# Kernel tuning notes

Measured on AMD Instinct MI355X. Metric: run time of the kernel, lower is better.

The kernel has to match this reference:

```python
import jax, jax.numpy as jnp
import numpy as np

H, HD, RD = 16, 128, 64          # n_heads, head_dim, rope_dim
CD = HD - RD                      # content_dim = 64
THETA = 10000.0


def apply_rope(x, cos, sin):
    # x: [B,H,T,RD]; cos/sin: [T,RD//2] broadcast over B,H
    d = x.shape[-1] // 2
    x1, x2 = x[..., :d], x[..., d:]
    return jnp.concatenate([x1 * cos - x2 * sin, x1 * sin + x2 * cos], axis=-1)


def setup_inputs() -> dict:
    key = jax.random.key(0)
    ks = jax.random.split(key, 9)
    d_model, q_rank, d_latent = 2048, 512, 512
    B, T = 2, 2048
    s = 0.02
    return {
        "x": jax.random.normal(ks[0], (B, T, d_model), dtype=jnp.float32),
        "Wq_down": jax.random.normal(ks[1], (d_model, q_rank), dtype=jnp.float32) * s,
        "Wq_up": jax.random.normal(ks[2], (q_rank, H * CD), dtype=jnp.float32) * s,
        "Wq_rope": jax.random.normal(ks[3], (d_model, H * RD), dtype=jnp.float32) * s,
        "Wkv_down": jax.random.normal(ks[4], (d_model, d_latent), dtype=jnp.float32) * s,
        "Wk_up": jax.random.normal(ks[5], (d_latent, H * CD), dtype=jnp.float32) * s,
        "Wv_up": jax.random.normal(ks[6], (d_latent, H * HD), dtype=jnp.float32) * s,
        "Wk_rope": jax.random.normal(ks[7], (d_model, H * RD), dtype=jnp.float32) * s,
        "Wo": jax.random.normal(ks[8], (H * HD, d_model), dtype=jnp.float32) * s,
    }


def reference(x, Wq_down, Wq_up, Wq_rope, Wkv_down, Wk_up, Wv_up, Wk_rope, Wo):
    B, T, _ = x.shape

    # low-rank projections
    q_content = (x @ Wq_down) @ Wq_up            # [B,T,H*CD]
    q_pos = x @ Wq_rope                          # [B,T,H*RD]
    kv_latent = x @ Wkv_down                     # [B,T,d_latent]
    k_content = kv_latent @ Wk_up                # [B,T,H*CD]
    k_pos = x @ Wk_rope                          # [B,T,H*RD]
    v = kv_latent @ Wv_up                        # [B,T,H*HD]

    def split_heads(t, d):
        return t.reshape(B, T, H, d).transpose(0, 2, 1, 3)  # [B,H,T,d]

    q_content = split_heads(q_content, CD)
    q_pos = split_heads(q_pos, RD)
    k_content = split_heads(k_content, CD)
    k_pos = split_heads(k_pos, RD)
    v = split_heads(v, HD)

    # rotary tables: [T, RD//2]
    inv_freq = 1.0 / (THETA ** (jnp.arange(0, RD, 2, dtype=jnp.float32) / RD))
    freqs = jnp.arange(T, dtype=jnp.float32)[:, None] * inv_freq[None, :]
    cos, sin = jnp.cos(freqs), jnp.sin(freqs)

    q_pos = apply_rope(q_pos, cos, sin)
    k_pos = apply_rope(k_pos, cos, sin)

    q = jnp.concatenate([q_content, q_pos], axis=-1)  # [B,H,T,HD]
    k = jnp.concatenate([k_content, k_pos], axis=-1)  # [B,H,T,HD]

    # causal SDPA, scale = 1/sqrt(head_dim)
    scale = 1.0 / jnp.sqrt(jnp.asarray(HD, dtype=q.dtype))
    scores = jnp.einsum("bhqd,bhkd->bhqk", q, k) * scale
    causal = jnp.tril(jnp.ones((T, T), dtype=bool))
    scores = jnp.where(causal, scores, jnp.finfo(scores.dtype).min)
    attn = jax.nn.softmax(scores, axis=-1)
    out = jnp.einsum("bhqk,bhkd->bhqd", attn, v)      # [B,H,T,HD]

    out = out.transpose(0, 2, 1, 3).reshape(B, T, H * HD)
    return out @ Wo
```

## Files before the change

kernel.cpp:

```cpp
#include <hip/hip_runtime.h>
#include <hip/hip_bf16.h>
#include <stdint.h>
#include <math.h>

#define H_ 16
#define HD_ 128
#define RD_ 64
#define CD_ 64
#define DM_ 2048
#define QR_ 512
#define DL_ 512
#define B_ 2
#define T_ 2048
#define M_TOT (B_*T_)

typedef __attribute__((ext_vector_type(8))) short short8;
typedef __attribute__((ext_vector_type(4))) float f32x4;
typedef __attribute__((ext_vector_type(16))) float f32x16;

__device__ __forceinline__ unsigned short f2b_hw(float f){
  __hip_bfloat16 h = __float2bfloat16(f);
  union { __hip_bfloat16 h; unsigned short u; } c; c.h = h; return c.u;
}
__device__ __forceinline__ float b2f(unsigned short b){
  union { unsigned u; float f; } a; a.u = ((unsigned)b) << 16;
  return a.f;
}
__device__ __forceinline__ unsigned pack2(float lo, float hi){
  __hip_bfloat162 h2 = __float22bfloat162_rn(make_float2(lo, hi));
  union { __hip_bfloat162 h; unsigned u; } c; c.h = h2; return c.u;
}

#define GLOAD16(g, l) __builtin_amdgcn_global_load_lds( \
    (__attribute__((address_space(1))) void*)(g), \
    (__attribute__((address_space(3))) void*)(l), 16, 0, 0)

__global__ void cast_f32_bf16(const float* __restrict__ src,
                              unsigned short* __restrict__ dst, int n,
                              float2* __restrict__ tab){
  int bid = blockIdx.x;
  if (bid >= 8192) {
    int idx = (bid - 8192) * 256 + threadIdx.x;
    int t = idx >> 5, j = idx & 31;
    float invf = exp2f(-(float)j * 0.4152410118750f);
    float fr = (float)t * invf;
    float s, c;
    sincosf(fr, &s, &c);
    tab[idx] = make_float2(c, s);
    return;
  }
  int i = (bid * 256 + threadIdx.x) * 4;
  if (i < n){
    float4 v = *(const float4*)(src + i);
    ushort4 o;
    o.x = f2b_hw(v.x); o.y = f2b_hw(v.y); o.z = f2b_hw(v.z); o.w = f2b_hw(v.w);
    *(ushort4*)(dst + i) = o;
  }
}

struct TTe { const float* src; unsigned short* dst; int K, N, blk0; };
struct TT8 { TTe e[8]; };

__global__ void transpose_cast8(TT8 tab){
  __shared__ float tile[32][33];
  int bid = blockIdx.x;
  const float* src = tab.e[0].src;
  unsigned short* dst = tab.e[0].dst;
  int K = tab.e[0].K, N = tab.e[0].N, loc = bid;
  #pragma unroll
  for (int j = 1; j < 8; j++){
    if (bid >= tab.e[j].blk0){
      src = tab.e[j].src; dst = tab.e[j].dst;
      K = tab.e[j].K; N = tab.e[j].N; loc = bid - tab.e[j].blk0;
    }
  }
  int cols = N / 32;
  int n0 = (loc % cols) * 32, k0 = (loc / cols) * 32;
  int tx = threadIdx.x, ty = threadIdx.y;
  float4 v = *(const float4*)&src[(size_t)(k0 + ty) * N + n0 + tx * 4];
  tile[ty][tx * 4 + 0] = v.x;
  tile[ty][tx * 4 + 1] = v.y;
  tile[ty][tx * 4 + 2] = v.z;
  tile[ty][tx * 4 + 3] = v.w;
  __syncthreads();
  ushort4 o;
  o.x = f2b_hw(tile[tx * 4 + 0][ty]);
  o.y = f2b_hw(tile[tx * 4 + 1][ty]);
  o.z = f2b_hw(tile[tx * 4 + 2][ty]);
  o.w = f2b_hw(tile[tx * 4 + 3][ty]);
  *(ushort4*)&dst[(size_t)(n0 + ty) * K + k0 + tx * 4] = o;
}

template<int MODE>
__global__ __launch_bounds__(512, 1) void gemm256(
    const unsigned short* __restrict__ A, int lda,
    const unsigned short* __restrict__ Bt,
    void* __restrict__ Cv, void* __restrict__ Cv2, void* __restrict__ Cv3,
    const float2* __restrict__ tab,
    int ldc, int N, int K)
{
  __shared__ __align__(16) unsigned short lds[65536];
  char* ldsb = (char*)lds;

  const int tid = threadIdx.x;
  const int lane = tid & 63, w = tid >> 6;
  const int wm = w >> 2, wn = w & 3;
  const int l15 = lane & 15, kg = lane >> 4;

  int gx = gridDim.x;
  int nwg = gx * gridDim.y;
  int lin = blockIdx.x + gx * blockIdx.y;
  int q8 = nwg >> 3;
  int nl = (lin & 7) * q8 + (lin >> 3);
  int m0 = (nl / gx) * 256, n0 = (nl % gx) * 256;

  const unsigned short* Aeff = A;
  if (MODE == 5 && n0 >= 1024) Aeff = A + 512;

  const int srow = tid >> 3;
  const int scol = ((((tid & 7) << 4) ^ (((tid >> 5) & 1) << 5)) >> 1);
  const int aswz = ((l15 >> 2) & 1) << 5;

#define STG(bufb, kt) do {                                                     \
    int k0_ = (kt) * 64;                                                       \
    _Pragma("unroll")                                                          \
    for (int h_ = 0; h_ < 2; h_++)                                             \
      _Pragma("unroll")                                                        \
      for (int i_ = 0; i_ < 2; i_++) {                                         \
        GLOAD16(Aeff + (size_t)(m0 + h_*128 + i_*64 + srow) * lda + k0_ + scol,\
                ldsb + (bufb)*65536 + h_*16384 + i_*8192 + tid*16);            \
        GLOAD16(Bt + (size_t)(n0 + h_*128 + i_*64 + srow) * K + k0_ + scol,    \
                ldsb + (bufb)*65536 + 32768 + h_*16384 + i_*8192 + tid*16);    \
      }                                                                        \
  } while (0)

  f32x4 acc[8][4];
  #pragma unroll
  for (int i = 0; i < 8; i++)
    #pragma unroll
    for (int j = 0; j < 4; j++)
      acc[i][j] = (f32x4){0.f, 0.f, 0.f, 0.f};

  const int nK = K >> 6;
  STG(0, 0);
  STG(1, 1);

  for (int t = 0; t < nK; t++) {
    const int c = t & 1;
    if (t < nK - 1) { asm volatile("s_waitcnt vmcnt(8)" ::: "memory"); }
    else            { asm volatile("s_waitcnt vmcnt(0)" ::: "memory"); }
    __builtin_amdgcn_s_barrier();
    __builtin_amdgcn_sched_barrier(0);

    const char* bufA = ldsb + c * 65536 + wm * 16384;
    const char* bufB = ldsb + c * 65536 + 32768;

    short8 bfr[4][2];
    #pragma unroll
    for (int nf = 0; nf < 4; nf++) {
      int nr = wn * 64 + nf * 16 + l15;
      #pragma unroll
      for (int kk = 0; kk < 2; kk++) {
        int L = (nr & 127) * 128 + kk * 64 + kg * 16;
        bfr[nf][kk] = *(const short8*)(bufB + (nr >> 7) * 16384 + (L ^ aswz));
      }
    }
    __builtin_amdgcn_s_setprio(1);
    #pragma unroll
    for (int mh = 0; mh < 2; mh++) {
      short8 afr[4][2];
      #pragma unroll
      for (int q = 0; q < 4; q++) {
        int mf = mh * 4 + q;
        #pragma unroll
        for (int kk = 0; kk < 2; kk++) {
          int L = (mf * 16 + l15) * 128 + kk * 64 + kg * 16;
          afr[q][kk] = *(const short8*)(bufA + (L ^ aswz));
        }
      }
      #pragma unroll
      for (int q = 0; q < 4; q++)
        #pragma unroll
        for (int nf = 0; nf < 4; nf++)
          #pragma unroll
          for (int kk = 0; kk < 2; kk++)
            acc[mh*4+q][nf] = __builtin_amdgcn_mfma_f32_16x16x32_bf16(
                afr[q][kk], bfr[nf][kk], acc[mh*4+q][nf], 0, 0, 0);
    }
    __builtin_amdgcn_s_setprio(0);
    __builtin_amdgcn_sched_barrier(0);
    __builtin_amdgcn_s_barrier();
    __builtin_amdgcn_sched_barrier(0);
    if (t + 2 < nK) STG(c, t + 2);
  }
#undef STG

  if (MODE == 4) {
    if (n0 < 1024) {
      unsigned short* C = (unsigned short*)Cv;
      #pragma unroll
      for (int mf = 0; mf < 8; mf++)
        #pragma unroll
        for (int nf = 0; nf < 4; nf++)
          #pragma unroll
          for (int rr = 0; rr < 4; rr++) {
            int row = m0 + wm * 128 + mf * 16 + kg * 4 + rr;
            int col = n0 + wn * 64 + nf * 16 + l15;
            C[(size_t)row * ldc + col] = f2b_hw(acc[mf][nf][rr]);
          }
    } else {
      const bool isq = (n0 < 2048);
      unsigned short* dst = (unsigned short*)(isq ? Cv2 : Cv3);
      int hbase = ((n0 - (isq ? 1024 : 2048)) >> 6) + wn;
      #pragma unroll
      for (int nf = 0; nf < 2; nf++) {
        int jr = nf * 16 + l15;
        #pragma unroll
        for (int mf = 0; mf < 8; mf++)
          #pragma unroll
          for (int rr = 0; rr < 4; rr++) {
            int gr = m0 + wm * 128 + mf * 16 + kg * 4 + rr;
            int tt = gr & (T_ - 1), bb = gr >> 11;
            float2 cs = tab[tt * 32 + jr];
            float x1 = acc[mf][nf][rr], x2 = acc[mf][nf + 2][rr];
            size_t base = ((size_t)(bb * H_ + hbase) * T_ + tt) * 128 + 64;
            dst[base + jr]      = f2b_hw(x1 * cs.x - x2 * cs.y);
            dst[base + jr + 32] = f2b_hw(x1 * cs.y + x2 * cs.x);
          }
      }
    }
  } else {
    if (n0 < 2048) {
      unsigned short* dstp = (unsigned short*)(n0 < 1024 ? Cv : Cv2);
      int cb0 = n0 - (n0 < 1024 ? 0 : 1024);
      #pragma unroll
      for (int nf = 0; nf < 4; nf++) {
        int colb = cb0 + wn * 64 + nf * 16 + l15;
        int h = colb >> 6, d = colb & 63;
        #pragma unroll
        for (int mf = 0; mf < 8; mf++)
          #pragma unroll
          for (int rr = 0; rr < 4; rr++) {
            int gr = m0 + wm * 128 + mf * 16 + kg * 4 + rr;
            size_t idx = ((size_t)((gr >> 11) * H_ + h) * T_ + (gr & (T_-1))) * 128 + d;
            dstp[idx] = f2b_hw(acc[mf][nf][rr]);
          }
      }
    } else {
      unsigned short* vtp = (unsigned short*)Cv3;
      #pragma unroll
      for (int nf = 0; nf < 4; nf++) {
        int c2 = n0 + wn * 64 + nf * 16 + l15 - 2048;
        int h = c2 >> 7, d = c2 & 127;
        #pragma unroll
        for (int mf = 0; mf < 8; mf++) {
          int gr0 = m0 + wm * 128 + mf * 16 + kg * 4;
          int bb = gr0 >> 11, t0 = gr0 & (T_-1);
          ushort4 o;
          o.x = f2b_hw(acc[mf][nf][0]); o.y = f2b_hw(acc[mf][nf][1]);
          o.z = f2b_hw(acc[mf][nf][2]); o.w = f2b_hw(acc[mf][nf][3]);
          *(ushort4*)&vtp[((size_t)(bb * H_ + h) * 128 + d) * T_ + t0] = o;
        }
      }
    }
  }
}

__global__ __launch_bounds__(512, 1) void gemm_out(
    const unsigned short* __restrict__ A, int lda,
    const unsigned short* __restrict__ Bt,
    float* __restrict__ C, int ldc, int K)
{
  __shared__ __align__(16) unsigned short lds[49152];
  char* ldsb = (char*)lds;

  const int tid = threadIdx.x;
  const int lane = tid & 63, w = tid >> 6;
  const int wm = w >> 2, wn = w & 3;
  const int l15 = lane & 15, kg = lane >> 4;

  int gx = gridDim.x;
  int nwg = gx * gridDim.y;
  int lin = blockIdx.x + gx * blockIdx.y;
  int q8 = nwg >> 3;
  int nl = (lin & 7) * q8 + (lin >> 3);
  int m0 = (nl / gx) * 128, n0 = (nl % gx) * 256;

  const int srow = tid >> 3;
  const int scol = ((((tid & 7) << 4) ^ (((tid >> 5) & 1) << 5)) >> 1);
  const int aswz = ((l15 >> 2) & 1) << 5;

#define STG(bufb, kt) do {                                                     \
    int k0_ = (kt) * 64;                                                       \
    _Pragma("unroll")                                                          \
    for (int i_ = 0; i_ < 2; i_++)                                             \
      GLOAD16(A + (size_t)(m0 + i_*64 + srow) * lda + k0_ + scol,              \
              ldsb + (bufb)*49152 + i_*8192 + tid*16);                         \
    _Pragma("unroll")                                                          \
    for (int i_ = 0; i_ < 4; i_++)                                             \
      GLOAD16(Bt + (size_t)(n0 + i_*64 + srow) * K + k0_ + scol,               \
              ldsb + (bufb)*49152 + 16384 + i_*8192 + tid*16);                 \
  } while (0)

  f32x4 acc[4][4];
  #pragma unroll
  for (int i = 0; i < 4; i++)
    #pragma unroll
    for (int j = 0; j < 4; j++)
      acc[i][j] = (f32x4){0.f, 0.f, 0.f, 0.f};

  const int nK = K >> 6;
  STG(0, 0);
  STG(1, 1);

  for (int t = 0; t < nK; t++) {
    const int c = t & 1;
    if (t < nK - 1) { asm volatile("s_waitcnt vmcnt(6)" ::: "memory"); }
    else            { asm volatile("s_waitcnt vmcnt(0)" ::: "memory"); }
    __builtin_amdgcn_s_barrier();
    __builtin_amdgcn_sched_barrier(0);

    const char* bufA = ldsb + c * 49152 + wm * 8192;
    const char* bufB = ldsb + c * 49152 + 16384;

    short8 bfr[4][2];
    #pragma unroll
    for (int nf = 0; nf < 4; nf++) {
      int nr = wn * 64 + nf * 16 + l15;
      #pragma unroll
      for (int kk = 0; kk < 2; kk++) {
        int L = (nr & 63) * 128 + kk * 64 + kg * 16;
        bfr[nf][kk] = *(const short8*)(bufB + (nr >> 6) * 8192 + (L ^ aswz));
      }
    }
    short8 afr[4][2];
    #pragma unroll
    for (int mf = 0; mf < 4; mf++)
      #pragma unroll
      for (int kk = 0; kk < 2; kk++) {
        int L = (mf * 16 + l15) * 128 + kk * 64 + kg * 16;
        afr[mf][kk] = *(const short8*)(bufA + (L ^ aswz));
      }
    __builtin_amdgcn_s_setprio(1);
    #pragma unroll
    for (int mf = 0; mf < 4; mf++)
      #pragma unroll
      for (int nf = 0; nf < 4; nf++)
        #pragma unroll
        for (int kk = 0; kk < 2; kk++)
          acc[mf][nf] = __builtin_amdgcn_mfma_f32_16x16x32_bf16(
              afr[mf][kk], bfr[nf][kk], acc[mf][nf], 0, 0, 0);
    __builtin_amdgcn_s_setprio(0);
    __builtin_amdgcn_sched_barrier(0);
    __builtin_amdgcn_s_barrier();
    __builtin_amdgcn_sched_barrier(0);
    if (t + 2 < nK) STG(c, t + 2);
  }
#undef STG

  #pragma unroll
  for (int mf = 0; mf < 4; mf++)
    #pragma unroll
    for (int nf = 0; nf < 4; nf++)
      #pragma unroll
      for (int rr = 0; rr < 4; rr++) {
        int row = m0 + wm * 64 + mf * 16 + kg * 4 + rr;
        int col = n0 + wn * 64 + nf * 16 + l15;
        C[(size_t)row * ldc + col] = acc[mf][nf][rr];
      }
}

__global__ __launch_bounds__(256, 2) void attn_fwd8(
    const unsigned short* __restrict__ qh,
    const unsigned short* __restrict__ kh,
    const unsigned short* __restrict__ vt,
    unsigned short* __restrict__ ao)
{
  __shared__ __align__(16) unsigned short lds[4 * 8192];

  const int tid  = threadIdx.x;
  const int lane = tid & 63, w = tid >> 6;
  const int l31  = lane & 31, hi = lane >> 5;
  const int bh = blockIdx.y;
  const int b  = bh >> 4, hd = bh & 15;
  int qt = blockIdx.x;
  if (bh >= 16) qt = 15 - qt;
  const int q0w   = qt * 128 + w * 32;
  const int qg    = q0w + l31;
  const int qmaxw = q0w + 31;
  const int nt    = 2 * qt + 2;

  const unsigned short* Qg = qh + (size_t)bh * T_ * 128;
  const unsigned short* Kg = kh + (size_t)bh * T_ * 128;
  const unsigned short* Vg = vt + (size_t)bh * 128 * T_;

  short8 qf[8];
  #pragma unroll
  for (int kc = 0; kc < 8; kc++)
    qf[kc] = *(const short8*)&Qg[(size_t)qg * 128 + kc * 16 + hi * 8];

  f32x16 accO[4];
  #pragma unroll
  for (int sb = 0; sb < 4; sb++)
    #pragma unroll
    for (int r = 0; r < 16; r++) accO[sb][r] = 0.f;

  float m = -1e30f, lsum = 0.f;
  const float SC = 0.12751743f;

  int krow[4], kwof[4], vrow[4], vwof[4];
  #pragma unroll
  for (int jj = 0; jj < 4; jj++){
    int r_ = (w * 4 + jj) * 4 + (lane >> 4);
    krow[jj] = r_;
    kwof[jj] = r_ * 128 + ((((lane & 15) * 16) ^ ((r_ & 7) << 4)) >> 1);
    int d_ = (w * 4 + jj) * 8 + (lane >> 3);
    vrow[jj] = d_;
    vwof[jj] = d_ * 64 + ((((lane & 7) * 16) ^ ((d_ & 7) << 4)) >> 1);
  }
  const int kcol = (lane & 15) * 8;
  const int vcol = (lane & 7) * 8;

  uint4 kst[4], vst[4];

#define REG_LOAD(kvt) do {                                                    \
    int kv0s = (kvt) * 64;                                                    \
    _Pragma("unroll")                                                         \
    for (int j_ = 0; j_ < 4; j_++) {                                          \
      kst[j_] = *(const uint4*)&Kg[(size_t)(kv0s + krow[j_]) * 128 + kcol];   \
      vst[j_] = *(const uint4*)&Vg[(size_t)vrow[j_] * T_ + kv0s + vcol];      \
    }                                                                         \
  } while (0)

#define DS_WRITE(bufi) do {                                                   \
    unsigned short* ksb_ = lds + (bufi) * 8192;                               \
    unsigned short* vsb_ = lds + 16384 + (bufi) * 8192;                       \
    _Pragma("unroll")                                                         \
    for (int j_ = 0; j_ < 4; j_++) {                                          \
      *(uint4*)&ksb_[kwof[j_]] = kst[j_];                                     \
      *(uint4*)&vsb_[vwof[j_]] = vst[j_];                                     \
    }                                                                         \
  } while (0)

  REG_LOAD(0);
  DS_WRITE(0);
  if (nt > 1) REG_LOAD(1);
  asm volatile("s_waitcnt lgkmcnt(0)" ::: "memory");
  __builtin_amdgcn_s_barrier();
  __builtin_amdgcn_sched_barrier(0);

  for (int t = 0; t < nt; t++) {
    const int cur = t & 1;
    if (t + 1 < nt) DS_WRITE(cur ^ 1);
    if (t + 2 < nt) REG_LOAD(t + 2);
    const int kv0 = t * 64;
    if (kv0 <= qmaxw) {
      const unsigned short* Kb = lds + cur * 8192;
      const unsigned short* Vb = lds + 16384 + cur * 8192;

      f32x16 sa0, sa1, sb0, sb1;
      #pragma unroll
      for (int r = 0; r < 16; r++) { sa0[r] = 0.f; sa1[r] = 0.f; sb0[r] = 0.f; sb1[r] = 0.f; }
      __builtin_amdgcn_s_setprio(1);
      #pragma unroll
      for (int kc = 0; kc < 8; kc += 2) {
        int co0 = (kc * 32 + hi * 16);
        int co1 = ((kc + 1) * 32 + hi * 16);
        int r0 = l31, r1 = 32 + l31;
        short8 kf0a = *(const short8*)&Kb[r0 * 128 + ((co0 ^ ((r0 & 7) << 4)) >> 1)];
        short8 kf1a = *(const short8*)&Kb[r1 * 128 + ((co0 ^ ((r1 & 7) << 4)) >> 1)];
        short8 kf0b = *(const short8*)&Kb[r0 * 128 + ((co1 ^ ((r0 & 7) << 4)) >> 1)];
        short8 kf1b = *(const short8*)&Kb[r1 * 128 + ((co1 ^ ((r1 & 7) << 4)) >> 1)];
        sa0 = __builtin_amdgcn_mfma_f32_32x32x16_bf16(kf0a, qf[kc], sa0, 0, 0, 0);
        sa1 = __builtin_amdgcn_mfma_f32_32x32x16_bf16(kf1a, qf[kc], sa1, 0, 0, 0);
        sb0 = __builtin_amdgcn_mfma_f32_32x32x16_bf16(kf0b, qf[kc + 1], sb0, 0, 0, 0);
        sb1 = __builtin_amdgcn_mfma_f32_32x32x16_bf16(kf1b, qf[kc + 1], sb1, 0, 0, 0);
      }
      __builtin_amdgcn_s_setprio(0);
      sa0 += sb0;
      sa1 += sb1;

      float p0[16], p1[16];
      float pmax = -1e30f;
      bool needMask = (kv0 + 63 > q0w);
      if (needMask) {
        #pragma unroll
        for (int r = 0; r < 16; r++) {
          int crow = (r & 3) + 8 * (r >> 2) + 4 * hi;
          float v0 = sa0[r] * SC;
          float v1 = sa1[r] * SC;
          if (kv0 + crow > qg)      v0 = -1e30f;
          if (kv0 + 32 + crow > qg) v1 = -1e30f;
          p0[r] = v0; p1[r] = v1;
          pmax = fmaxf(pmax, fmaxf(v0, v1));
        }
      } else {
        #pragma unroll
        for (int r = 0; r < 16; r++) {
          float v0 = sa0[r] * SC;
          float v1 = sa1[r] * SC;
          p0[r] = v0; p1[r] = v1;
          pmax = fmaxf(pmax, fmaxf(v0, v1));
        }
      }
      pmax = fmaxf(pmax, __shfl_xor(pmax, 32, 64));
      if (!__all(pmax <= m + 8.f)) {
        float mn  = fmaxf(m, pmax);
        float fac = exp2f(m - mn);
        m = mn;
        lsum *= fac;
        #pragma unroll
        for (int sb = 0; sb < 4; sb++)
          #pragma unroll
          for (int r = 0; r < 16; r++) accO[sb][r] *= fac;
      }
      float ls = 0.f;
      #pragma unroll
      for (int r = 0; r < 16; r++) {
        p0[r] = exp2f(p0[r] - m);
        p1[r] = exp2f(p1[r] - m);
        ls += p0[r] + p1[r];
      }
      ls += __shfl_xor(ls, 32, 64);
      lsum += ls;

      #pragma unroll
      for (int kc2 = 0; kc2 < 4; kc2++) {
        unsigned A01, A23, B01, B23;
        if (kc2 == 0) { A01 = pack2(p0[0], p0[1]);  A23 = pack2(p0[2], p0[3]);
                        B01 = pack2(p0[4], p0[5]);  B23 = pack2(p0[6], p0[7]); }
        else if (kc2 == 1) { A01 = pack2(p0[8], p0[9]);   A23 = pack2(p0[10], p0[11]);
                             B01 = pack2(p0[12], p0[13]); B23 = pack2(p0[14], p0[15]); }
        else if (kc2 == 2) { A01 = pack2(p1[0], p1[1]);  A23 = pack2(p1[2], p1[3]);
                             B01 = pack2(p1[4], p1[5]);  B23 = pack2(p1[6], p1[7]); }
        else { A01 = pack2(p1[8], p1[9]);   A23 = pack2(p1[10], p1[11]);
               B01 = pack2(p1[12], p1[13]); B23 = pack2(p1[14], p1[15]); }
        asm("v_permlane32_swap_b32 %0, %1" : "+v"(A01), "+v"(B01));
        asm("v_permlane32_swap_b32 %0, %1" : "+v"(A23), "+v"(B23));
        union { unsigned u[4]; short8 v; } pk;
        pk.u[0] = A01; pk.u[1] = A23; pk.u[2] = B01; pk.u[3] = B23;
        short8 pa = pk.v;
        __builtin_amdgcn_s_setprio(1);
        #pragma unroll
        for (int sb = 0; sb < 4; sb++) {
          int d = sb * 32 + l31;
          short8 vf = *(const short8*)&Vb[d * 64 + (((kc2 * 32 + hi * 16) ^ ((d & 7) << 4)) >> 1)];
          accO[sb] = __builtin_amdgcn_mfma_f32_32x32x16_bf16(vf, pa, accO[sb], 0, 0, 0);
        }
        __builtin_amdgcn_s_setprio(0);
      }
    }
    __builtin_amdgcn_sched_barrier(0);
    asm volatile("s_waitcnt lgkmcnt(0)" ::: "memory");
    __builtin_amdgcn_s_barrier();
    __builtin_amdgcn_sched_barrier(0);
  }

  float rl = 1.0f / lsum;
  size_t orow = ((size_t)b * T_ + qg) * (H_*HD_) + hd * 128;
  #pragma unroll
  for (int sb = 0; sb < 4; sb++)
    #pragma unroll
    for (int g = 0; g < 4; g++) {
      ushort4 o;
      o.x = f2b_hw(accO[sb][4 * g + 0] * rl);
      o.y = f2b_hw(accO[sb][4 * g + 1] * rl);
      o.z = f2b_hw(accO[sb][4 * g + 2] * rl);
      o.w = f2b_hw(accO[sb][4 * g + 3] * rl);
      *(ushort4*)&ao[orow + sb * 32 + 8 * g + 4 * hi] = o;
    }
#undef REG_LOAD
#undef DS_WRITE
}

extern "C" void kernel_launch(void* const* d_in, const int* in_sizes, int n_in,
                              void* d_out, int out_size, void* d_ws, size_t ws_size,
                              hipStream_t stream)
{
  (void)in_sizes; (void)n_in; (void)out_size; (void)ws_size;
  const float* x        = (const float*)d_in[0];
  const float* Wq_down  = (const float*)d_in[1];
  const float* Wq_up    = (const float*)d_in[2];
  const float* Wq_rope  = (const float*)d_in[3];
  const float* Wkv_down = (const float*)d_in[4];
  const float* Wk_up    = (const float*)d_in[5];
  const float* Wv_up    = (const float*)d_in[6];
  const float* Wk_rope  = (const float*)d_in[7];
  const float* Wo       = (const float*)d_in[8];

  char* ws = (char*)d_ws;
  unsigned short* xb      = (unsigned short*)(ws + 0);
  unsigned short* Wdall   = (unsigned short*)(ws + 16777216);
  unsigned short* WquT    = (unsigned short*)(ws + 29360128);
  unsigned short* WkcvT   = (unsigned short*)(ws + 30408704);
  unsigned short* WoT     = (unsigned short*)(ws + 33554432);
  unsigned short* projall = (unsigned short*)(ws + 41943040);
  unsigned short* qh      = (unsigned short*)(ws + 67108864);
  unsigned short* kh      = (unsigned short*)(ws + 83886080);
  unsigned short* vt      = (unsigned short*)(ws + 100663296);
  unsigned short* ao      = (unsigned short*)(ws + 117440512);
  float2*         ctab    = (float2*)(ws + 134217728);

  cast_f32_bf16<<<8192 + 256, 256, 0, stream>>>(x, xb, M_TOT * DM_, ctab);

  TT8 tab;
  int blk = 0;
  tab.e[0] = { Wq_down,  Wdall,               DM_, QR_,     blk }; blk += (QR_/32)*(DM_/32);
  tab.e[1] = { Wkv_down, Wdall + 512*2048,    DM_, DL_,     blk }; blk += (DL_/32)*(DM_/32);
  tab.e[2] = { Wq_rope,  Wdall + 1024*2048,   DM_, H_*RD_,  blk }; blk += (H_*RD_/32)*(DM_/32);
  tab.e[3] = { Wk_rope,  Wdall + 2048*2048,   DM_, H_*RD_,  blk }; blk += (H_*RD_/32)*(DM_/32);
  tab.e[4] = { Wq_up,    WquT,                QR_, H_*CD_,  blk }; blk += (H_*CD_/32)*(QR_/32);
  tab.e[5] = { Wk_up,    WkcvT,               DL_, H_*CD_,  blk }; blk += (H_*CD_/32)*(DL_/32);
  tab.e[6] = { Wv_up,    WkcvT + 1024*512,    DL_, H_*HD_,  blk }; blk += (H_*HD_/32)*(DL_/32);
  tab.e[7] = { Wo,       WoT,                 H_*HD_, DM_,  blk }; blk += (DM_/32)*(H_*HD_/32);
  transpose_cast8<<<blk, dim3(8, 32), 0, stream>>>(tab);

  gemm256<4><<<dim3(3072/256, M_TOT/256), 512, 0, stream>>>(
      xb, DM_, Wdall, projall, qh, kh, ctab, 1024, 3072, DM_);
  gemm256<5><<<dim3(4096/256, M_TOT/256), 512, 0, stream>>>(
      projall, 1024, WquT, qh, kh, vt, nullptr, 0, 4096, DL_);

  attn_fwd8<<<dim3(16, 32), 256, 0, stream>>>(qh, kh, vt, ao);

  gemm_out<<<dim3(DM_/256, M_TOT/128), 512, 0, stream>>>(
      ao, 2048, WoT, (float*)d_out, DM_, H_*HD_);
}
```

Measured before the change: 292.4 us.

## Merge prep kernels into one launch and fold softmax scale into Q

Combines the input cast/rope-table kernel and the weight transpose-cast kernel into a single launch with block-range dispatch, removing one kernel launch and its tail. Also applies the attention scale (including log2e) to Q content and rope parts in the projection GEMM epilogues, so the attention loop no longer multiplies every score. Pre-scaling Q before bf16 rounding slightly changes numerics.

Result: no change. 290.4 us (median of 3 runs) (-0.7%).

```diff
diff --git a/kernel.cpp b/kernel.cpp
--- a/kernel.cpp
+++ b/kernel.cpp
@@ -35,12 +35,27 @@
     (__attribute__((address_space(1))) void*)(g), \
     (__attribute__((address_space(3))) void*)(l), 16, 0, 0)
 
-__global__ void cast_f32_bf16(const float* __restrict__ src,
-                              unsigned short* __restrict__ dst, int n,
-                              float2* __restrict__ tab){
+struct TTe { const float* src; unsigned short* dst; int K, N, blk0; };
+struct TT8 { TTe e[8]; };
+
+__global__ void prep_all(const float* __restrict__ src,
+                         unsigned short* __restrict__ dst, int n,
+                         float2* __restrict__ tab, TT8 tt){
+  __shared__ float tile[32][33];
   int bid = blockIdx.x;
-  if (bid >= 8192) {
-    int idx = (bid - 8192) * 256 + threadIdx.x;
+  int tid = threadIdx.x;
+  if (bid < 8192) {
+    int i = (bid * 256 + tid) * 4;
+    if (i < n){
+      float4 v = *(const float4*)(src + i);
+      ushort4 o;
+      o.x = f2b_hw(v.x); o.y = f2b_hw(v.y); o.z = f2b_hw(v.z); o.w = f2b_hw(v.w);
+      *(ushort4*)(dst + i) = o;
+    }
+    return;
+  }
+  if (bid < 8448) {
+    int idx = (bid - 8192) * 256 + tid;
     int t = idx >> 5, j = idx & 31;
     float invf = exp2f(-(float)j * 0.4152410118750f);
     float fr = (float)t * invf;
@@ -49,35 +64,21 @@
     tab[idx] = make_float2(c, s);
     return;
   }
-  int i = (bid * 256 + threadIdx.x) * 4;
-  if (i < n){
-    float4 v = *(const float4*)(src + i);
-    ushort4 o;
-    o.x = f2b_hw(v.x); o.y = f2b_hw(v.y); o.z = f2b_hw(v.z); o.w = f2b_hw(v.w);
-    *(ushort4*)(dst + i) = o;
-  }
-}
-
-struct TTe { const float* src; unsigned short* dst; int K, N, blk0; };
-struct TT8 { TTe e[8]; };
-
-__global__ void transpose_cast8(TT8 tab){
-  __shared__ float tile[32][33];
-  int bid = blockIdx.x;
-  const float* src = tab.e[0].src;
-  unsigned short* dst = tab.e[0].dst;
-  int K = tab.e[0].K, N = tab.e[0].N, loc = bid;
+  int loc = bid - 8448;
+  const float* wsrc = tt.e[0].src;
+  unsigned short* wdst = tt.e[0].dst;
+  int K = tt.e[0].K, N = tt.e[0].N, l2 = loc;
   #pragma unroll
   for (int j = 1; j < 8; j++){
-    if (bid >= tab.e[j].blk0){
-      src = tab.e[j].src; dst = tab.e[j].dst;
-      K = tab.e[j].K; N = tab.e[j].N; loc = bid - tab.e[j].blk0;
+    if (loc >= tt.e[j].blk0){
+      wsrc = tt.e[j].src; wdst = tt.e[j].dst;
+      K = tt.e[j].K; N = tt.e[j].N; l2 = loc - tt.e[j].blk0;
     }
   }
   int cols = N / 32;
-  int n0 = (loc % cols) * 32, k0 = (loc / cols) * 32;
-  int tx = threadIdx.x, ty = threadIdx.y;
-  float4 v = *(const float4*)&src[(size_t)(k0 + ty) * N + n0 + tx * 4];
+  int n0 = (l2 % cols) * 32, k0 = (l2 / cols) * 32;
+  int tx = tid & 7, ty = tid >> 3;
+  float4 v = *(const float4*)&wsrc[(size_t)(k0 + ty) * N + n0 + tx * 4];
   tile[ty][tx * 4 + 0] = v.x;
   tile[ty][tx * 4 + 1] = v.y;
   tile[ty][tx * 4 + 2] = v.z;
@@ -88,7 +89,7 @@
   o.y = f2b_hw(tile[tx * 4 + 1][ty]);
   o.z = f2b_hw(tile[tx * 4 + 2][ty]);
   o.w = f2b_hw(tile[tx * 4 + 3][ty]);
-  *(ushort4*)&dst[(size_t)(n0 + ty) * K + k0 + tx * 4] = o;
+  *(ushort4*)&wdst[(size_t)(n0 + ty) * K + k0 + tx * 4] = o;
 }
 
 template<int MODE>
@@ -211,6 +212,7 @@
     } else {
       const bool isq = (n0 < 2048);
       unsigned short* dst = (unsigned short*)(isq ? Cv2 : Cv3);
+      const float qsc = isq ? 0.12751743f : 1.0f;
       int hbase = ((n0 - (isq ? 1024 : 2048)) >> 6) + wn;
       #pragma unroll
       for (int nf = 0; nf < 2; nf++) {
@@ -224,14 +226,15 @@
             float2 cs = tab[tt * 32 + jr];
             float x1 = acc[mf][nf][rr], x2 = acc[mf][nf + 2][rr];
             size_t base = ((size_t)(bb * H_ + hbase) * T_ + tt) * 128 + 64;
-            dst[base + jr]      = f2b_hw(x1 * cs.x - x2 * cs.y);
-            dst[base + jr + 32] = f2b_hw(x1 * cs.y + x2 * cs.x);
+            dst[base + jr]      = f2b_hw((x1 * cs.x - x2 * cs.y) * qsc);
+            dst[base + jr + 32] = f2b_hw((x1 * cs.y + x2 * cs.x) * qsc);
           }
       }
     }
   } else {
     if (n0 < 2048) {
       unsigned short* dstp = (unsigned short*)(n0 < 1024 ? Cv : Cv2);
+      const float qsc = (n0 < 1024) ? 0.12751743f : 1.0f;
       int cb0 = n0 - (n0 < 1024 ? 0 : 1024);
       #pragma unroll
       for (int nf = 0; nf < 4; nf++) {
@@ -243,7 +246,7 @@
           for (int rr = 0; rr < 4; rr++) {
             int gr = m0 + wm * 128 + mf * 16 + kg * 4 + rr;
             size_t idx = ((size_t)((gr >> 11) * H_ + h) * T_ + (gr & (T_-1))) * 128 + d;
-            dstp[idx] = f2b_hw(acc[mf][nf][rr]);
+            dstp[idx] = f2b_hw(acc[mf][nf][rr] * qsc);
           }
       }
     } else {
@@ -406,7 +409,6 @@
     for (int r = 0; r < 16; r++) accO[sb][r] = 0.f;
 
   float m = -1e30f, lsum = 0.f;
-  const float SC = 0.12751743f;
 
   int krow[4], kwof[4], vrow[4], vwof[4];
   #pragma unroll
@@ -487,8 +489,8 @@
         #pragma unroll
         for (int r = 0; r < 16; r++) {
           int crow = (r & 3) + 8 * (r >> 2) + 4 * hi;
-          float v0 = sa0[r] * SC;
-          float v1 = sa1[r] * SC;
+          float v0 = sa0[r];
+          float v1 = sa1[r];
           if (kv0 + crow > qg)      v0 = -1e30f;
           if (kv0 + 32 + crow > qg) v1 = -1e30f;
           p0[r] = v0; p1[r] = v1;
@@ -497,8 +499,8 @@
       } else {
         #pragma unroll
         for (int r = 0; r < 16; r++) {
-          float v0 = sa0[r] * SC;
-          float v1 = sa1[r] * SC;
+          float v0 = sa0[r];
+          float v1 = sa1[r];
           p0[r] = v0; p1[r] = v1;
           pmax = fmaxf(pmax, fmaxf(v0, v1));
         }
@@ -601,8 +603,6 @@
   unsigned short* ao      = (unsigned short*)(ws + 117440512);
   float2*         ctab    = (float2*)(ws + 134217728);
 
-  cast_f32_bf16<<<8192 + 256, 256, 0, stream>>>(x, xb, M_TOT * DM_, ctab);
-
   TT8 tab;
   int blk = 0;
   tab.e[0] = { Wq_down,  Wdall,               DM_, QR_,     blk }; blk += (QR_/32)*(DM_/32);
@@ -613,7 +613,8 @@
   tab.e[5] = { Wk_up,    WkcvT,               DL_, H_*CD_,  blk }; blk += (H_*CD_/32)*(DL_/32);
   tab.e[6] = { Wv_up,    WkcvT + 1024*512,    DL_, H_*HD_,  blk }; blk += (H_*HD_/32)*(DL_/32);
   tab.e[7] = { Wo,       WoT,                 H_*HD_, DM_,  blk }; blk += (DM_/32)*(H_*HD_/32);
-  transpose_cast8<<<blk, dim3(8, 32), 0, stream>>>(tab);
+
+  prep_all<<<8192 + 256 + blk, 256, 0, stream>>>(x, xb, M_TOT * DM_, ctab, tab);
 
   gemm256<4><<<dim3(3072/256, M_TOT/256), 512, 0, stream>>>(
       xb, DM_, Wdall, projall, qh, kh, ctab, 1024, 3072, DM_);
```
